# Kernel tuning notes

Hardware: AMD Instinct MI355X
Metric: run time of the kernel (lower is better)

The kernel has to match this reference:

```python
import jax, jax.numpy as jnp
import numpy as np

DIM_IN = 512
DIM_HEAD = 64
HEADS = 8
KV_HEADS = 2
CONTEXT_LEN = 4096
B, N = 4, 2048


def setup_inputs() -> dict:
    key = jax.random.key(0)
    ks = jax.random.split(key, 6)
    s = 1.0 / np.sqrt(DIM_IN)
    return {
        "x": jax.random.normal(ks[0], (B, DIM_IN, N), dtype=jnp.float32),
        "gamma": jnp.ones((DIM_IN,), jnp.float32),
        "beta": jnp.zeros((DIM_IN,), jnp.float32),
        "Wq": jax.random.normal(ks[1], (DIM_IN, DIM_HEAD * HEADS), jnp.float32) * s,
        "Wkv": jax.random.normal(ks[2], (DIM_IN, DIM_HEAD * KV_HEADS * 2), jnp.float32) * s,
        "Wout": jax.random.normal(ks[3], (DIM_HEAD * HEADS, DIM_IN), jnp.float32) * (1.0 / np.sqrt(DIM_HEAD * HEADS)),
        "bout": jnp.zeros((DIM_IN,), jnp.float32),
    }


def _rotate_half(t):
    t1, t2 = jnp.split(t, 2, axis=-1)
    return jnp.concatenate([-t2, t1], axis=-1)


def _xpos_rotary(q, k, n, dim_head, scale_base):
    # lucidrains-style xPos rotary embedding
    pos = jnp.arange(n, dtype=jnp.float32)
    inv_freq = 1.0 / (10000.0 ** (jnp.arange(0, dim_head, 2, dtype=jnp.float32) / dim_head))
    freqs = pos[:, None] * inv_freq[None, :]            # (n, dh/2)
    freqs = jnp.concatenate([freqs, freqs], axis=-1)    # (n, dh)
    base_scale = (jnp.arange(0, dim_head, 2, dtype=jnp.float32) + 0.4 * dim_head) / (1.4 * dim_head)
    power = (pos - n // 2) / scale_base                 # (n,)
    scale = base_scale[None, :] ** power[:, None]       # (n, dh/2)
    scale = jnp.concatenate([scale, scale], axis=-1)    # (n, dh)
    cos, sin = jnp.cos(freqs), jnp.sin(freqs)
    q = (q * cos + _rotate_half(q) * sin) * scale
    k = (k * cos + _rotate_half(k) * sin) / scale
    return q, k


def reference(x, gamma, beta, Wq, Wkv, Wout, bout):
    b, d, n = x.shape
    h, kvh, dh = HEADS, KV_HEADS, DIM_HEAD
    xt = jnp.swapaxes(x, 1, 2)                           # (b, n, d)
    mu = jnp.mean(xt, axis=-1, keepdims=True)
    var = jnp.mean((xt - mu) ** 2, axis=-1, keepdims=True)
    xn = (xt - mu) * jax.lax.rsqrt(var + 1e-5) * gamma + beta
    q = (xn @ Wq).reshape(b, n, h, dh).transpose(0, 2, 1, 3)      # (b, h, n, dh)
    kv = xn @ Wkv
    k, v = jnp.split(kv, 2, axis=-1)
    k = k.reshape(b, n, kvh, dh).transpose(0, 2, 1, 3)            # (b, kvh, n, dh)
    v = v.reshape(b, n, kvh, dh).transpose(0, 2, 1, 3)
    r = h // kvh
    # repeat 'b h n d -> b (r h) n d': tile whole kv-head block r times
    k = jnp.tile(k, (1, r, 1, 1))
    v = jnp.tile(v, (1, r, 1, 1))
    q, k = _xpos_rotary(q, k, n, dh, CONTEXT_LEN)
    scores = jnp.einsum("bhqd,bhkd->bhqk", q, k) * (1.0 / np.sqrt(dh))
    attn = jax.nn.softmax(scores, axis=-1)
    out = jnp.einsum("bhqk,bhkd->bhqd", attn, v)                  # (b, h, n, dh)
    out = out.transpose(0, 2, 1, 3).reshape(b, n, h * dh)
    y = xn + out @ Wout + bout                                    # residual uses normed x
    return jnp.swapaxes(y, 1, 2)                                  # (b, d, n)
```

## Files before the change

### kernel.cpp

```cpp
#include <hip/hip_runtime.h>
#include <stdint.h>

#define DIM 512
#define DH  64
#define NH  8
#define NKV 2
#define NB  4
#define NS  2048
#define TAB (NS*32)

typedef __attribute__((ext_vector_type(8))) short short8;
typedef __attribute__((ext_vector_type(4))) short s16x4;
typedef __attribute__((ext_vector_type(4))) float f32x4;
typedef __attribute__((ext_vector_type(16))) float f32x16;
typedef __attribute__((ext_vector_type(2))) unsigned uint2v;
typedef __attribute__((ext_vector_type(4))) unsigned uint4v;

__device__ __forceinline__ unsigned short f2bf(float f) {
  union { float f; unsigned u; } v; v.f = f;
  return (unsigned short)((v.u + 0x7fffu + ((v.u >> 16) & 1u)) >> 16);
}
__device__ __forceinline__ float bf2f(unsigned short b) {
  union { unsigned u; float f; } v; v.u = ((unsigned)b) << 16;
  return v.f;
}
__device__ __forceinline__ unsigned cvt_pk_bf16(float a, float b) {
  unsigned r;
  asm("v_cvt_pk_bf16_f32 %0, %1, %2" : "=v"(r) : "v"(a), "v"(b));
  return r;
}
__device__ __forceinline__ float exp2_raw(float x) {
  float r;
  asm("v_exp_f32 %0, %1" : "=v"(r) : "v"(x));
  return r;
}
__device__ __forceinline__ float rcp_raw(float x) {
  float r;
  asm("v_rcp_f32 %0, %1" : "=v"(r) : "v"(x));
  return r;
}
__device__ __forceinline__ short8 merge8(short8 a, short8 b, float rl) {
  uint4v u;
  #pragma unroll
  for (int i = 0; i < 4; ++i) {
    float x0 = (bf2f((unsigned short)a[2*i])   + bf2f((unsigned short)b[2*i]))   * rl;
    float x1 = (bf2f((unsigned short)a[2*i+1]) + bf2f((unsigned short)b[2*i+1])) * rl;
    u[i] = cvt_pk_bf16(x0, x1);
  }
  return __builtin_bit_cast(short8, u);
}

__global__ __launch_bounds__(256) void lnprep_kernel(const float* __restrict__ x,
    const float* __restrict__ gamma, const float* __restrict__ beta,
    const float* __restrict__ Wq, const float* __restrict__ Wkv, const float* __restrict__ Wout,
    unsigned short* __restrict__ xn, unsigned short* __restrict__ Wqkvt,
    unsigned short* __restrict__ Woutt, float* __restrict__ tabs) {
  __shared__ float t[64][65];
  const int gid = blockIdx.x;
  const int tid = threadIdx.x;
  if (gid < 256) {
    const int b = gid >> 6;
    const int n0 = (gid & 63) * 32;
    const int nl = tid & 31, grp = tid >> 5;
    const float* xb = x + (size_t)b * DIM * NS + (size_t)grp * 64 * NS + n0 + nl;
    float v[64];
    float s = 0.f, s2 = 0.f;
    #pragma unroll
    for (int i = 0; i < 64; ++i) {
      v[i] = xb[(size_t)i * NS];
      s += v[i]; s2 += v[i] * v[i];
    }
    float* sm = &t[0][0];
    float* sq = &t[8][0];
    float* mu_s = &t[16][0];
    float* rs_s = &t[17][0];
    sm[grp*32 + nl] = s; sq[grp*32 + nl] = s2;
    __syncthreads();
    if (tid < 32) {
      float ts = 0.f, ts2 = 0.f;
      #pragma unroll
      for (int g = 0; g < 8; ++g) { ts += sm[g*32 + tid]; ts2 += sq[g*32 + tid]; }
      float mu = ts * (1.f/512.f);
      float var = ts2 * (1.f/512.f) - mu*mu;
      mu_s[tid] = mu; rs_s[tid] = rsqrtf(var + 1e-5f);
    }
    __syncthreads();
    const float mu = mu_s[nl], rs = rs_s[nl];
    unsigned short* dst = &xn[((size_t)(b*NS + n0 + nl))*DIM + grp*64];
    #pragma unroll
    for (int c = 0; c < 8; ++c) {
      short8 o;
      #pragma unroll
      for (int j = 0; j < 8; ++j) {
        int d = grp*64 + c*8 + j;
        o[j] = (short)f2bf((v[c*8 + j] - mu) * rs * gamma[d] + beta[d]);
      }
      *(short8*)&dst[c*8] = o;
    }
    return;
  }
  const int id = gid - 256;
  if (id >= 160) {
    int base = (id - 160) * 256 + tid;
    #pragma unroll 4
    for (int ii = 0; ii < 32; ++ii) {
      int tix = base + ii * 2048;
      int pos = tix >> 5, i = tix & 31;
      float inv = exp2f(-(float)i * (13.287712379549449f / 32.f));
      float ang = (float)pos * inv;
      float sv, cv; sincosf(ang, &sv, &cv);
      float bse = ((float)(2*i) + 25.6f) / 89.6f;
      float power = ((float)pos - 1024.f) / 4096.f;
      float sc = exp2f(power * log2f(bse));
      tabs[tix]         = cv;
      tabs[TAB + tix]   = sv;
      tabs[2*TAB + tix] = sc * 0.125f * 1.4426950408889634f;
      tabs[3*TAB + tix] = 1.f / sc;
    }
    return;
  }
  const float* src; int W, k0, c0; unsigned short* dst; int drow0;
  if (id < 64)      { src = Wq;  W = 512; k0 = (id>>3)*64;        c0 = (id&7)*64;        dst = Wqkvt; drow0 = c0; }
  else if (id < 96) { int i2 = id-64; src = Wkv; W = 256; k0 = (i2>>2)*64; c0 = (i2&3)*64; dst = Wqkvt; drow0 = 512 + c0; }
  else              { int i3 = id-96; src = Wout; W = 512; k0 = (i3>>3)*64; c0 = (i3&7)*64; dst = Woutt; drow0 = c0; }
  #pragma unroll 4
  for (int it = 0; it < 16; ++it) {
    int row = it*4 + (tid>>6), col = tid & 63;
    t[row][col] = src[(size_t)(k0+row)*W + c0 + col];
  }
  __syncthreads();
  #pragma unroll 4
  for (int it = 0; it < 16; ++it) {
    int row = it*4 + (tid>>6), col = tid & 63;
    dst[(size_t)(drow0 + row)*512 + k0 + col] = f2bf(t[col][row]);
  }
}

__global__ __launch_bounds__(256, 3) void qkv_kernel(const unsigned short* __restrict__ A,
    const unsigned short* __restrict__ Bt, const float* __restrict__ tabs,
    unsigned short* __restrict__ q, unsigned short* __restrict__ k,
    unsigned short* __restrict__ v) {
  __shared__ __align__(16) short As[2][64][40];
  __shared__ __align__(16) short Bs[2][128][40];
  const int m0 = blockIdx.x * 64, ntile = blockIdx.y, n0 = ntile * 128;
  const int tid = threadIdx.x, w = tid >> 6, lane = tid & 63;
  const int wr = w >> 1, wc = w & 1;
  f32x4 acc[2][4];
  #pragma unroll
  for (int i = 0; i < 2; ++i)
    #pragma unroll
    for (int j = 0; j < 4; ++j) acc[i][j] = (f32x4){0.f,0.f,0.f,0.f};
  const int rA = tid >> 2, c8 = (tid & 3) * 8;
  const unsigned short* Ar0 = &A[(size_t)(m0 + rA)*DIM + c8];
  const unsigned short* Br0 = &Bt[(size_t)(n0 + rA)*DIM + c8];
  const unsigned short* Br1 = &Bt[(size_t)(n0 + 64 + rA)*DIM + c8];
  *(short8*)&As[0][rA][c8]      = *(const short8*)Ar0;
  *(short8*)&Bs[0][rA][c8]      = *(const short8*)Br0;
  *(short8*)&Bs[0][64 + rA][c8] = *(const short8*)Br1;
  short8 pa0 = *(const short8*)(Ar0 + 32);
  short8 pb0 = *(const short8*)(Br0 + 32);
  short8 pb1 = *(const short8*)(Br1 + 32);
  __syncthreads();
  for (int t = 0; t < 16; ++t) {
    const int cur = t & 1;
    short8 af[2], bfr[4];
    #pragma unroll
    for (int mf = 0; mf < 2; ++mf)
      af[mf] = *(const short8*)&As[cur][wr*32 + mf*16 + (lane & 15)][(lane >> 4)*8];
    #pragma unroll
    for (int nf = 0; nf < 4; ++nf)
      bfr[nf] = *(const short8*)&Bs[cur][wc*64 + nf*16 + (lane & 15)][(lane >> 4)*8];
    __builtin_amdgcn_s_setprio(1);
    #pragma unroll
    for (int mf = 0; mf < 2; ++mf)
      #pragma unroll
      for (int nf = 0; nf < 4; ++nf)
        acc[mf][nf] = __builtin_amdgcn_mfma_f32_16x16x32_bf16(af[mf], bfr[nf], acc[mf][nf], 0, 0, 0);
    __builtin_amdgcn_s_setprio(0);
    if (t < 15) {
      *(short8*)&As[cur^1][rA][c8]      = pa0;
      *(short8*)&Bs[cur^1][rA][c8]      = pb0;
      *(short8*)&Bs[cur^1][64 + rA][c8] = pb1;
      if (t < 14) {
        const int kc = (t + 2) * 32;
        pa0 = *(const short8*)(Ar0 + kc);
        pb0 = *(const short8*)(Br0 + kc);
        pb1 = *(const short8*)(Br1 + kc);
      }
      __syncthreads();
    }
  }
  const int mw = m0 + wr*32, cw = n0 + wc*64;
  if (ntile < 4) {
    #pragma unroll
    for (int nfp = 0; nfp < 2; ++nfp) {
      const int c_lo = cw + nfp*16 + (lane & 15);
      const int head = c_lo >> 6, ii = c_lo & 31;
      const float* tb = tabs + ii;
      #pragma unroll
      for (int mf = 0; mf < 2; ++mf) {
        #pragma unroll
        for (int r = 0; r < 4; ++r) {
          int mm = mw + mf*16 + (lane >> 4)*4 + r;
          int bb = mm >> 11, n = mm & (NS-1);
          float cv = tb[n*32], sv = tb[TAB + n*32], qs = tb[2*TAB + n*32];
          float lo = acc[mf][nfp][r], hi = acc[mf][nfp+2][r];
          size_t base = (((size_t)bb*NH + head)*NS + n)*DH;
          q[base + ii]      = f2bf((lo*cv - hi*sv)*qs);
          q[base + ii + 32] = f2bf((hi*cv + lo*sv)*qs);
        }
      }
    }
  } else if (ntile == 4) {
    #pragma unroll
    for (int nfp = 0; nfp < 2; ++nfp) {
      const int c_lo = cw + nfp*16 + (lane & 15);
      const int kvh = (c_lo - 512) >> 6, ii = c_lo & 31;
      const float* tb = tabs + ii;
      #pragma unroll
      for (int mf = 0; mf < 2; ++mf) {
        #pragma unroll
        for (int r = 0; r < 4; ++r) {
          int mm = mw + mf*16 + (lane >> 4)*4 + r;
          int bb = mm >> 11, n = mm & (NS-1);
          float cv = tb[n*32], sv = tb[TAB + n*32], ks = tb[3*TAB + n*32];
          float lo = acc[mf][nfp][r], hi = acc[mf][nfp+2][r];
          size_t base = (((size_t)bb*NKV + kvh)*NS + n)*DH;
          k[base + ii]      = f2bf((lo*cv - hi*sv)*ks);
          k[base + ii + 32] = f2bf((hi*cv + lo*sv)*ks);
        }
      }
    }
  } else {
    #pragma unroll
    for (int nf = 0; nf < 4; ++nf) {
      const int c = cw + nf*16 + (lane & 15);
      const int rel = c - 640;
      const int kvh = rel >> 6, dd = rel & 63;
      #pragma unroll
      for (int mf = 0; mf < 2; ++mf) {
        int mm = mw + mf*16 + (lane >> 4)*4;
        int bb = mm >> 11, n = mm & (NS-1);
        s16x4 sv4;
        #pragma unroll
        for (int r = 0; r < 4; ++r) sv4[r] = (short)f2bf(acc[mf][nf][r]);
        *(s16x4*)&v[(((size_t)bb*NKV + kvh)*DH + dd)*NS + n] = sv4;
      }
    }
  }
}

__global__ __launch_bounds__(512, 2) void attn_kernel(const unsigned short* __restrict__ q,
    const unsigned short* __restrict__ kg, const unsigned short* __restrict__ vtp,
    unsigned short* __restrict__ op0, unsigned short* __restrict__ op1,
    float* __restrict__ lp) {
  __shared__ __align__(16) short kt[2][64][72];
  __shared__ __align__(16) short vt[2][64][72];
  const int bid = blockIdx.x;
  const int dsr = (bid & 7) * 64 + (bid >> 3);
  const int qt   = dsr & 7;
  const int half = (dsr >> 3) & 1;
  const int bh   = dsr >> 4;
  const int h = bh & 7, b = bh >> 3;
  const int kvh = h & (NKV-1);
  const int q0 = qt * 256;
  const int tid = threadIdx.x, w = tid >> 6, lane = tid & 63;
  const int l31 = lane & 31, hf = lane >> 5;
  short8 q8[4];
  const unsigned short* qp = q + (((size_t)b*NH + h)*NS + q0 + w*32 + l31)*DH + hf*8;
  #pragma unroll
  for (int s = 0; s < 4; ++s) q8[s] = *(const short8*)(qp + s*16);
  const unsigned short* kb = kg + ((size_t)b*NKV + kvh)*NS*DH;
  const unsigned short* vb = vtp + ((size_t)b*NKV + kvh)*DH*NS;
  const int kbase = half * 1024;
  const int srow = tid >> 3, scol = (tid & 7) * 8;
  *(short8*)&kt[0][srow][scol] = *(const short8*)&kb[(size_t)(kbase + srow)*DH + scol];
  *(short8*)&vt[0][srow][scol] = *(const short8*)&vb[(size_t)srow*NS + kbase + scol];
  short8 kr = *(const short8*)&kb[(size_t)(kbase + 64 + srow)*DH + scol];
  short8 vr = *(const short8*)&vb[(size_t)srow*NS + kbase + 64 + scol];
  f32x16 o0 = {}, o1 = {};
  float lsum = 0.f;
  __syncthreads();
  for (int t = 0; t < 16; ++t) {
    const int cur = t & 1;
    short8 kf0[4], kf1[4];
    #pragma unroll
    for (int s = 0; s < 4; ++s) {
      kf0[s] = *(const short8*)&kt[cur][l31][s*16 + hf*8];
      kf1[s] = *(const short8*)&kt[cur][32 + l31][s*16 + hf*8];
    }
    f32x16 st0 = {}, st1 = {};
    __builtin_amdgcn_s_setprio(1);
    #pragma unroll
    for (int s = 0; s < 4; ++s) {
      st0 = __builtin_amdgcn_mfma_f32_32x32x16_bf16(kf0[s], q8[s], st0, 0, 0, 0);
      st1 = __builtin_amdgcn_mfma_f32_32x32x16_bf16(kf1[s], q8[s], st1, 0, 0, 0);
    }
    __builtin_amdgcn_s_setprio(0);
    float p0[16], p1[16];
    #pragma unroll
    for (int r = 0; r < 16; ++r) {
      p0[r] = exp2_raw(st0[r]);
      p1[r] = exp2_raw(st1[r]);
      lsum += p0[r] + p1[r];
    }
    short8 paf[4];
    #pragma unroll
    for (int t2 = 0; t2 < 2; ++t2) {
      const float* pp = t2 ? p1 : p0;
      #pragma unroll
      for (int w16 = 0; w16 < 2; ++w16) {
        const int rb = w16*8;
        unsigned x = cvt_pk_bf16(pp[rb+0], pp[rb+1]);
        unsigned z = cvt_pk_bf16(pp[rb+2], pp[rb+3]);
        unsigned y = cvt_pk_bf16(pp[rb+4], pp[rb+5]);
        unsigned u = cvt_pk_bf16(pp[rb+6], pp[rb+7]);
        uint2v r1 = __builtin_amdgcn_permlane32_swap(x, y, false, false);
        uint2v r2 = __builtin_amdgcn_permlane32_swap(z, u, false, false);
        uint4v pk4;
        pk4[0] = r1[0]; pk4[1] = r2[0]; pk4[2] = r1[1]; pk4[3] = r2[1];
        paf[t2*2 + w16] = __builtin_bit_cast(short8, pk4);
      }
    }
    __builtin_amdgcn_s_setprio(1);
    #pragma unroll
    for (int kwin = 0; kwin < 4; ++kwin) {
      short8 vf0 = *(const short8*)&vt[cur][l31][kwin*16 + hf*8];
      short8 vf1 = *(const short8*)&vt[cur][32 + l31][kwin*16 + hf*8];
      o0 = __builtin_amdgcn_mfma_f32_32x32x16_bf16(paf[kwin], vf0, o0, 0, 0, 0);
      o1 = __builtin_amdgcn_mfma_f32_32x32x16_bf16(paf[kwin], vf1, o1, 0, 0, 0);
    }
    __builtin_amdgcn_s_setprio(0);
    if (t < 15) {
      *(short8*)&kt[cur^1][srow][scol] = kr;
      *(short8*)&vt[cur^1][srow][scol] = vr;
      if (t < 14) {
        const int k2 = kbase + (t + 2) * 64;
        kr = *(const short8*)&kb[(size_t)(k2 + srow)*DH + scol];
        vr = *(const short8*)&vb[(size_t)srow*NS + k2 + scol];
      }
      __syncthreads();
    }
  }
  lsum += __shfl_xor(lsum, 32);
  if (hf == 0)
    lp[(size_t)half*NB*NH*NS + ((size_t)b*NH + h)*NS + q0 + w*32 + l31] = lsum;
  unsigned short* op = half ? op1 : op0;
  #pragma unroll
  for (int r = 0; r < 16; ++r) {
    const int ql = (r & 3) + 8*(r >> 2) + 4*hf;
    const int n = q0 + w*32 + ql;
    unsigned short* aor = &op[((size_t)b*NS + n)*DIM + h*DH + l31];
    aor[0]  = f2bf(o0[r]);
    aor[32] = f2bf(o1[r]);
  }
}

__global__ __launch_bounds__(256, 3) void out_kernel(const unsigned short* __restrict__ op0,
    const unsigned short* __restrict__ op1, const float* __restrict__ lp,
    const unsigned short* __restrict__ Bt, const unsigned short* __restrict__ xn,
    const float* __restrict__ bout, float* __restrict__ out) {
  __shared__ __align__(16) short As[2][64][40];
  __shared__ __align__(16) short Bs[2][128][40];
  const int m0 = blockIdx.x * 64, n0 = blockIdx.y * 128;
  const int tid = threadIdx.x, w = tid >> 6, lane = tid & 63;
  const int wr = w >> 1, wc = w & 1;
  f32x4 acc[2][4];
  #pragma unroll
  for (int i = 0; i < 2; ++i)
    #pragma unroll
    for (int j = 0; j < 4; ++j) acc[i][j] = (f32x4){0.f,0.f,0.f,0.f};
  const int rA = tid >> 2, c8 = (tid & 3) * 8;
  const int rowm = m0 + rA;
  const int b0 = rowm >> 11, nn0 = rowm & (NS-1);
  const float* lp0 = lp + ((size_t)b0*NH)*NS + nn0;
  const float* lp1 = lp0 + (size_t)NB*NH*NS;
  const unsigned short* A0 = &op0[(size_t)rowm*DIM + c8];
  const unsigned short* A1 = &op1[(size_t)rowm*DIM + c8];
  const unsigned short* Br0 = &Bt[(size_t)(n0 + rA)*DIM + c8];
  const unsigned short* Br1 = &Bt[(size_t)(n0 + 64 + rA)*DIM + c8];
  float rlc = rcp_raw(lp0[0] + lp1[0]);
  *(short8*)&As[0][rA][c8]      = merge8(*(const short8*)A0, *(const short8*)A1, rlc);
  *(short8*)&Bs[0][rA][c8]      = *(const short8*)Br0;
  *(short8*)&Bs[0][64 + rA][c8] = *(const short8*)Br1;
  short8 pa0 = *(const short8*)(A0 + 32);
  short8 pa1 = *(const short8*)(A1 + 32);
  float rlp = rlc;
  short8 pb0 = *(const short8*)(Br0 + 32);
  short8 pb1 = *(const short8*)(Br1 + 32);
  __syncthreads();
  for (int t = 0; t < 16; ++t) {
    const int cur = t & 1;
    short8 af[2], bfr[4];
    #pragma unroll
    for (int mf = 0; mf < 2; ++mf)
      af[mf] = *(const short8*)&As[cur][wr*32 + mf*16 + (lane & 15)][(lane >> 4)*8];
    #pragma unroll
    for (int nf = 0; nf < 4; ++nf)
      bfr[nf] = *(const short8*)&Bs[cur][wc*64 + nf*16 + (lane & 15)][(lane >> 4)*8];
    __builtin_amdgcn_s_setprio(1);
    #pragma unroll
    for (int mf = 0; mf < 2; ++mf)
      #pragma unroll
      for (int nf = 0; nf < 4; ++nf)
        acc[mf][nf] = __builtin_amdgcn_mfma_f32_16x16x32_bf16(af[mf], bfr[nf], acc[mf][nf], 0, 0, 0);
    __builtin_amdgcn_s_setprio(0);
    if (t < 15) {
      *(short8*)&As[cur^1][rA][c8]      = merge8(pa0, pa1, rlp);
      *(short8*)&Bs[cur^1][rA][c8]      = pb0;
      *(short8*)&Bs[cur^1][64 + rA][c8] = pb1;
      if (t < 14) {
        const int kc = (t + 2) * 32;
        pa0 = *(const short8*)(A0 + kc);
        pa1 = *(const short8*)(A1 + kc);
        pb0 = *(const short8*)(Br0 + kc);
        pb1 = *(const short8*)(Br1 + kc);
        const int h2 = (t + 2) >> 1;
        rlp = rcp_raw(lp0[h2*NS] + lp1[h2*NS]);
      }
      __syncthreads();
    }
  }
  const int mw = m0 + wr*32, cw = n0 + wc*64;
  #pragma unroll
  for (int nf = 0; nf < 4; ++nf) {
    const int d = cw + nf*16 + (lane & 15);
    const float bo = bout[d];
    #pragma unroll
    for (int mf = 0; mf < 2; ++mf) {
      const int mb = mw + mf*16 + (lane >> 4)*4;
      const int bb = mb >> 11, n = mb & (NS-1);
      f32x4 res;
      #pragma unroll
      for (int r = 0; r < 4; ++r)
        res[r] = acc[mf][nf][r] + bf2f(xn[(size_t)(mb + r)*DIM + d]) + bo;
      *(f32x4*)&out[((size_t)bb*DIM + d)*NS + n] = res;
    }
  }
}

extern "C" void kernel_launch(void* const* d_in, const int* in_sizes, int n_in,
                              void* d_out, int out_size, void* d_ws, size_t ws_size,
                              hipStream_t stream) {
  (void)in_sizes; (void)n_in; (void)out_size; (void)ws_size;
  const float* x     = (const float*)d_in[0];
  const float* gamma = (const float*)d_in[1];
  const float* beta  = (const float*)d_in[2];
  const float* Wq    = (const float*)d_in[3];
  const float* Wkv   = (const float*)d_in[4];
  const float* Wout  = (const float*)d_in[5];
  const float* bout  = (const float*)d_in[6];
  float* out = (float*)d_out;
  char* ws = (char*)d_ws;
  unsigned short* xn    = (unsigned short*)(ws);
  unsigned short* qb    = (unsigned short*)(ws + (size_t)(8<<20));
  unsigned short* kb    = (unsigned short*)(ws + (size_t)(16<<20));
  unsigned short* vb    = (unsigned short*)(ws + (size_t)(18<<20));
  unsigned short* op0   = (unsigned short*)(ws + (size_t)(20<<20));
  unsigned short* op1   = (unsigned short*)(ws + (size_t)(28<<20));
  unsigned short* wqkvt = (unsigned short*)(ws + (size_t)(36<<20));
  unsigned short* woutt = (unsigned short*)(ws + (size_t)(36<<20) + 786432);
  float* tabs           = (float*)(ws + (size_t)(36<<20) + 786432 + 524288);
  float* lp             = (float*)(ws + (size_t)(36<<20) + 786432 + 524288 + 1048576);

  lnprep_kernel<<<dim3(424), dim3(256), 0, stream>>>(x, gamma, beta, Wq, Wkv, Wout,
                                                     xn, wqkvt, woutt, tabs);
  qkv_kernel<<<dim3(128, 6), dim3(256), 0, stream>>>(xn, wqkvt, tabs, qb, kb, vb);
  attn_kernel<<<dim3(512), dim3(512), 0, stream>>>(qb, kb, vb, op0, op1, lp);
  out_kernel<<<dim3(128, 4), dim3(256), 0, stream>>>(op0, op1, lp, woutt, xn, bout, out);
}
```

Measured before the change: 85.34 us.

## Split attention key range into four partitions and merge four partials in output GEMM

The attention kernel now splits each query tile's keys into four 512-key quarters instead of two halves. This doubles the block count to 1024, and each block loops 8 key tiles instead of 16. The output projection kernel merges four bf16 partial outputs and four row-sum partials before normalising. This adds more parallelism and shorter per-block latency, but costs extra workspace traffic for two more 8MB partial buffers and extra loads in the out kernel. The launch bound is raised to 8 blocks per CU, which may cap registers hard enough to cause spills.

```diff
diff --git a/kernel.cpp b/kernel.cpp
--- a/kernel.cpp
+++ b/kernel.cpp
@@ -39,12 +39,14 @@
   asm("v_rcp_f32 %0, %1" : "=v"(r) : "v"(x));
   return r;
 }
-__device__ __forceinline__ short8 merge8(short8 a, short8 b, float rl) {
+__device__ __forceinline__ short8 merge8x4(short8 a, short8 b, short8 c, short8 d, float rl) {
   uint4v u;
   #pragma unroll
   for (int i = 0; i < 4; ++i) {
-    float x0 = (bf2f((unsigned short)a[2*i])   + bf2f((unsigned short)b[2*i]))   * rl;
-    float x1 = (bf2f((unsigned short)a[2*i+1]) + bf2f((unsigned short)b[2*i+1])) * rl;
+    float x0 = ((bf2f((unsigned short)a[2*i])   + bf2f((unsigned short)b[2*i]))
+              + (bf2f((unsigned short)c[2*i])   + bf2f((unsigned short)d[2*i]))) * rl;
+    float x1 = ((bf2f((unsigned short)a[2*i+1]) + bf2f((unsigned short)b[2*i+1]))
+              + (bf2f((unsigned short)c[2*i+1]) + bf2f((unsigned short)d[2*i+1]))) * rl;
     u[i] = cvt_pk_bf16(x0, x1);
   }
   return __builtin_bit_cast(short8, u);
@@ -250,17 +252,18 @@
   }
 }
 
-__global__ __launch_bounds__(512, 2) void attn_kernel(const unsigned short* __restrict__ q,
+__global__ __launch_bounds__(512, 8) void attn_kernel(const unsigned short* __restrict__ q,
     const unsigned short* __restrict__ kg, const unsigned short* __restrict__ vtp,
     unsigned short* __restrict__ op0, unsigned short* __restrict__ op1,
+    unsigned short* __restrict__ op2, unsigned short* __restrict__ op3,
     float* __restrict__ lp) {
   __shared__ __align__(16) short kt[2][64][72];
   __shared__ __align__(16) short vt[2][64][72];
   const int bid = blockIdx.x;
-  const int dsr = (bid & 7) * 64 + (bid >> 3);
-  const int qt   = dsr & 7;
-  const int half = (dsr >> 3) & 1;
-  const int bh   = dsr >> 4;
+  const int dsr = (bid & 7) * 128 + (bid >> 3);
+  const int qt      = dsr & 7;
+  const int quarter = (dsr >> 3) & 3;
+  const int bh      = dsr >> 5;
   const int h = bh & 7, b = bh >> 3;
   const int kvh = h & (NKV-1);
   const int q0 = qt * 256;
@@ -272,7 +275,7 @@
   for (int s = 0; s < 4; ++s) q8[s] = *(const short8*)(qp + s*16);
   const unsigned short* kb = kg + ((size_t)b*NKV + kvh)*NS*DH;
   const unsigned short* vb = vtp + ((size_t)b*NKV + kvh)*DH*NS;
-  const int kbase = half * 1024;
+  const int kbase = quarter * 512;
   const int srow = tid >> 3, scol = (tid & 7) * 8;
   *(short8*)&kt[0][srow][scol] = *(const short8*)&kb[(size_t)(kbase + srow)*DH + scol];
   *(short8*)&vt[0][srow][scol] = *(const short8*)&vb[(size_t)srow*NS + kbase + scol];
@@ -281,7 +284,7 @@
   f32x16 o0 = {}, o1 = {};
   float lsum = 0.f;
   __syncthreads();
-  for (int t = 0; t < 16; ++t) {
+  for (int t = 0; t < 8; ++t) {
     const int cur = t & 1;
     short8 kf0[4], kf1[4];
     #pragma unroll
@@ -331,10 +334,10 @@
       o1 = __builtin_amdgcn_mfma_f32_32x32x16_bf16(paf[kwin], vf1, o1, 0, 0, 0);
     }
     __builtin_amdgcn_s_setprio(0);
-    if (t < 15) {
+    if (t < 7) {
       *(short8*)&kt[cur^1][srow][scol] = kr;
       *(short8*)&vt[cur^1][srow][scol] = vr;
-      if (t < 14) {
+      if (t < 6) {
         const int k2 = kbase + (t + 2) * 64;
         kr = *(const short8*)&kb[(size_t)(k2 + srow)*DH + scol];
         vr = *(const short8*)&vb[(size_t)srow*NS + k2 + scol];
@@ -344,8 +347,9 @@
   }
   lsum += __shfl_xor(lsum, 32);
   if (hf == 0)
-    lp[(size_t)half*NB*NH*NS + ((size_t)b*NH + h)*NS + q0 + w*32 + l31] = lsum;
-  unsigned short* op = half ? op1 : op0;
+    lp[(size_t)quarter*NB*NH*NS + ((size_t)b*NH + h)*NS + q0 + w*32 + l31] = lsum;
+  unsigned short* op = (quarter & 2) ? ((quarter & 1) ? op3 : op2)
+                                     : ((quarter & 1) ? op1 : op0);
   #pragma unroll
   for (int r = 0; r < 16; ++r) {
     const int ql = (r & 3) + 8*(r >> 2) + 4*hf;
@@ -357,7 +361,8 @@
 }
 
 __global__ __launch_bounds__(256, 3) void out_kernel(const unsigned short* __restrict__ op0,
-    const unsigned short* __restrict__ op1, const float* __restrict__ lp,
+    const unsigned short* __restrict__ op1, const unsigned short* __restrict__ op2,
+    const unsigned short* __restrict__ op3, const float* __restrict__ lp,
     const unsigned short* __restrict__ Bt, const unsigned short* __restrict__ xn,
     const float* __restrict__ bout, float* __restrict__ out) {
   __shared__ __align__(16) short As[2][64][40];
@@ -373,18 +378,23 @@
   const int rA = tid >> 2, c8 = (tid & 3) * 8;
   const int rowm = m0 + rA;
   const int b0 = rowm >> 11, nn0 = rowm & (NS-1);
+  const size_t lstride = (size_t)NB*NH*NS;
   const float* lp0 = lp + ((size_t)b0*NH)*NS + nn0;
-  const float* lp1 = lp0 + (size_t)NB*NH*NS;
   const unsigned short* A0 = &op0[(size_t)rowm*DIM + c8];
   const unsigned short* A1 = &op1[(size_t)rowm*DIM + c8];
+  const unsigned short* A2 = &op2[(size_t)rowm*DIM + c8];
+  const unsigned short* A3 = &op3[(size_t)rowm*DIM + c8];
   const unsigned short* Br0 = &Bt[(size_t)(n0 + rA)*DIM + c8];
   const unsigned short* Br1 = &Bt[(size_t)(n0 + 64 + rA)*DIM + c8];
-  float rlc = rcp_raw(lp0[0] + lp1[0]);
-  *(short8*)&As[0][rA][c8]      = merge8(*(const short8*)A0, *(const short8*)A1, rlc);
+  float rlc = rcp_raw(((lp0[0] + lp0[lstride]) + (lp0[2*lstride] + lp0[3*lstride])));
+  *(short8*)&As[0][rA][c8] = merge8x4(*(const short8*)A0, *(const short8*)A1,
+                                      *(const short8*)A2, *(const short8*)A3, rlc);
   *(short8*)&Bs[0][rA][c8]      = *(const short8*)Br0;
   *(short8*)&Bs[0][64 + rA][c8] = *(const short8*)Br1;
   short8 pa0 = *(const short8*)(A0 + 32);
   short8 pa1 = *(const short8*)(A1 + 32);
+  short8 pa2 = *(const short8*)(A2 + 32);
+  short8 pa3 = *(const short8*)(A3 + 32);
   float rlp = rlc;
   short8 pb0 = *(const short8*)(Br0 + 32);
   short8 pb1 = *(const short8*)(Br1 + 32);
@@ -406,17 +416,20 @@
         acc[mf][nf] = __builtin_amdgcn_mfma_f32_16x16x32_bf16(af[mf], bfr[nf], acc[mf][nf], 0, 0, 0);
     __builtin_amdgcn_s_setprio(0);
     if (t < 15) {
-      *(short8*)&As[cur^1][rA][c8]      = merge8(pa0, pa1, rlp);
+      *(short8*)&As[cur^1][rA][c8]      = merge8x4(pa0, pa1, pa2, pa3, rlp);
       *(short8*)&Bs[cur^1][rA][c8]      = pb0;
       *(short8*)&Bs[cur^1][64 + rA][c8] = pb1;
       if (t < 14) {
         const int kc = (t + 2) * 32;
         pa0 = *(const short8*)(A0 + kc);
         pa1 = *(const short8*)(A1 + kc);
+        pa2 = *(const short8*)(A2 + kc);
+        pa3 = *(const short8*)(A3 + kc);
         pb0 = *(const short8*)(Br0 + kc);
         pb1 = *(const short8*)(Br1 + kc);
         const int h2 = (t + 2) >> 1;
-        rlp = rcp_raw(lp0[h2*NS] + lp1[h2*NS]);
+        rlp = rcp_raw(((lp0[h2*NS] + lp0[h2*NS + lstride])
+                     + (lp0[h2*NS + 2*lstride] + lp0[h2*NS + 3*lstride])));
       }
       __syncthreads();
     }
@@ -458,14 +471,16 @@
   unsigned short* vb    = (unsigned short*)(ws + (size_t)(18<<20));
   unsigned short* op0   = (unsigned short*)(ws + (size_t)(20<<20));
   unsigned short* op1   = (unsigned short*)(ws + (size_t)(28<<20));
-  unsigned short* wqkvt = (unsigned short*)(ws + (size_t)(36<<20));
-  unsigned short* woutt = (unsigned short*)(ws + (size_t)(36<<20) + 786432);
-  float* tabs           = (float*)(ws + (size_t)(36<<20) + 786432 + 524288);
-  float* lp             = (float*)(ws + (size_t)(36<<20) + 786432 + 524288 + 1048576);
+  unsigned short* op2   = (unsigned short*)(ws + (size_t)(36<<20));
+  unsigned short* op3   = (unsigned short*)(ws + (size_t)(44<<20));
+  unsigned short* wqkvt = (unsigned short*)(ws + (size_t)(52<<20));
+  unsigned short* woutt = (unsigned short*)(ws + (size_t)(52<<20) + 786432);
+  float* tabs           = (float*)(ws + (size_t)(52<<20) + 786432 + 524288);
+  float* lp             = (float*)(ws + (size_t)(52<<20) + 786432 + 524288 + 1048576);
 
   lnprep_kernel<<<dim3(424), dim3(256), 0, stream>>>(x, gamma, beta, Wq, Wkv, Wout,
                                                      xn, wqkvt, woutt, tabs);
   qkv_kernel<<<dim3(128, 6), dim3(256), 0, stream>>>(xn, wqkvt, tabs, qb, kb, vb);
-  attn_kernel<<<dim3(512), dim3(512), 0, stream>>>(qb, kb, vb, op0, op1, lp);
-  out_kernel<<<dim3(128, 4), dim3(256), 0, stream>>>(op0, op1, lp, woutt, xn, bout, out);
-}
+  attn_kernel<<<dim3(1024), dim3(512), 0, stream>>>(qb, kb, vb, op0, op1, op2, op3, lp);
+  out_kernel<<<dim3(128, 4), dim3(256), 0, stream>>>(op0, op1, op2, op3, lp, woutt, xn, bout, out);
+}
```

New measurement: 329.3 us. +285.9%, slower.

## Pre-swizzle K/V into MFMA fragment layout and load directly from global

Applied to the files above, without the earlier changes.

The qkv kernel now writes K and V in a layout that already matches the MFMA operand fragments, so each lane reads contiguous 16-byte chunks. The attention kernel drops its LDS double-buffering and all __syncthreads, loading K/V fragments straight from global memory (L2-cached). Blocks shrink to 256 threads and the grid doubles to 1024, and the setprio hints are removed. This removes LDS traffic and barrier stalls, but each wave now re-reads K/V from cache and global load latency is exposed without explicit prefetch.

```diff
diff --git a/kernel.cpp b/kernel.cpp
--- a/kernel.cpp
+++ b/kernel.cpp
@@ -216,6 +216,7 @@
     for (int nfp = 0; nfp < 2; ++nfp) {
       const int c_lo = cw + nfp*16 + (lane & 15);
       const int kvh = (c_lo - 512) >> 6, ii = c_lo & 31;
+      const int s_lo = ii >> 4, hfk = (ii >> 3) & 1, e = ii & 7;
       const float* tb = tabs + ii;
       #pragma unroll
       for (int mf = 0; mf < 2; ++mf) {
@@ -225,9 +226,11 @@
           int bb = mm >> 11, n = mm & (NS-1);
           float cv = tb[n*32], sv = tb[TAB + n*32], ks = tb[3*TAB + n*32];
           float lo = acc[mf][nfp][r], hi = acc[mf][nfp+2][r];
-          size_t base = (((size_t)bb*NKV + kvh)*NS + n)*DH;
-          k[base + ii]      = f2bf((lo*cv - hi*sv)*ks);
-          k[base + ii + 32] = f2bf((hi*cv + lo*sv)*ks);
+          const int hb = bb*NKV + kvh;
+          size_t cbase = (((size_t)hb*32 + (n >> 6))*2 + ((n >> 5) & 1))*4;
+          size_t lanepart = (size_t)(hfk*32 + (n & 31))*8 + e;
+          k[(cbase + s_lo)*512 + lanepart]     = f2bf((lo*cv - hi*sv)*ks);
+          k[(cbase + s_lo + 2)*512 + lanepart] = f2bf((hi*cv + lo*sv)*ks);
         }
       }
     }
@@ -237,66 +240,64 @@
       const int c = cw + nf*16 + (lane & 15);
       const int rel = c - 640;
       const int kvh = rel >> 6, dd = rel & 63;
+      const int dh2 = dd >> 5, l31v = dd & 31;
       #pragma unroll
       for (int mf = 0; mf < 2; ++mf) {
         int mm = mw + mf*16 + (lane >> 4)*4;
         int bb = mm >> 11, n = mm & (NS-1);
+        const int hb = bb*NKV + kvh;
         s16x4 sv4;
         #pragma unroll
         for (int r = 0; r < 4; ++r) sv4[r] = (short)f2bf(acc[mf][nf][r]);
-        *(s16x4*)&v[(((size_t)bb*NKV + kvh)*DH + dd)*NS + n] = sv4;
-      }
-    }
-  }
-}
-
-__global__ __launch_bounds__(512, 2) void attn_kernel(const unsigned short* __restrict__ q,
-    const unsigned short* __restrict__ kg, const unsigned short* __restrict__ vtp,
+        size_t idx = (((((size_t)hb*32 + (n >> 6))*2 + dh2)*4 + ((n >> 4) & 3))*64
+                     + ((n >> 3) & 1)*32 + l31v)*8 + (n & 7);
+        *(s16x4*)&v[idx] = sv4;
+      }
+    }
+  }
+}
+
+__global__ __launch_bounds__(256) void attn_kernel(const unsigned short* __restrict__ q,
+    const unsigned short* __restrict__ kfb, const unsigned short* __restrict__ vfb,
     unsigned short* __restrict__ op0, unsigned short* __restrict__ op1,
     float* __restrict__ lp) {
-  __shared__ __align__(16) short kt[2][64][72];
-  __shared__ __align__(16) short vt[2][64][72];
   const int bid = blockIdx.x;
-  const int dsr = (bid & 7) * 64 + (bid >> 3);
-  const int qt   = dsr & 7;
-  const int half = (dsr >> 3) & 1;
-  const int bh   = dsr >> 4;
+  const int dsr = (bid & 7) * 128 + (bid >> 3);
+  const int qtile = dsr & 15;
+  const int half  = (dsr >> 4) & 1;
+  const int bh    = dsr >> 5;
   const int h = bh & 7, b = bh >> 3;
   const int kvh = h & (NKV-1);
-  const int q0 = qt * 256;
+  const int hb = b*NKV + kvh;
   const int tid = threadIdx.x, w = tid >> 6, lane = tid & 63;
   const int l31 = lane & 31, hf = lane >> 5;
+  const int q0 = qtile*128 + w*32;
   short8 q8[4];
-  const unsigned short* qp = q + (((size_t)b*NH + h)*NS + q0 + w*32 + l31)*DH + hf*8;
+  const unsigned short* qp = q + (((size_t)b*NH + h)*NS + q0 + l31)*DH + hf*8;
   #pragma unroll
   for (int s = 0; s < 4; ++s) q8[s] = *(const short8*)(qp + s*16);
-  const unsigned short* kb = kg + ((size_t)b*NKV + kvh)*NS*DH;
-  const unsigned short* vb = vtp + ((size_t)b*NKV + kvh)*DH*NS;
-  const int kbase = half * 1024;
-  const int srow = tid >> 3, scol = (tid & 7) * 8;
-  *(short8*)&kt[0][srow][scol] = *(const short8*)&kb[(size_t)(kbase + srow)*DH + scol];
-  *(short8*)&vt[0][srow][scol] = *(const short8*)&vb[(size_t)srow*NS + kbase + scol];
-  short8 kr = *(const short8*)&kb[(size_t)(kbase + 64 + srow)*DH + scol];
-  short8 vr = *(const short8*)&vb[(size_t)srow*NS + kbase + 64 + scol];
+  const unsigned short* kf_base = kfb + ((size_t)hb*32 + half*16)*4096 + lane*8;
+  const unsigned short* vf_base = vfb + ((size_t)hb*32 + half*16)*4096 + lane*8;
   f32x16 o0 = {}, o1 = {};
   float lsum = 0.f;
-  __syncthreads();
   for (int t = 0; t < 16; ++t) {
-    const int cur = t & 1;
+    const unsigned short* kc = kf_base + (size_t)t*4096;
+    const unsigned short* vc = vf_base + (size_t)t*4096;
     short8 kf0[4], kf1[4];
     #pragma unroll
     for (int s = 0; s < 4; ++s) {
-      kf0[s] = *(const short8*)&kt[cur][l31][s*16 + hf*8];
-      kf1[s] = *(const short8*)&kt[cur][32 + l31][s*16 + hf*8];
+      kf0[s] = *(const short8*)(kc + s*512);
+      kf1[s] = *(const short8*)(kc + (4 + s)*512);
     }
     f32x16 st0 = {}, st1 = {};
-    __builtin_amdgcn_s_setprio(1);
     #pragma unroll
     for (int s = 0; s < 4; ++s) {
       st0 = __builtin_amdgcn_mfma_f32_32x32x16_bf16(kf0[s], q8[s], st0, 0, 0, 0);
       st1 = __builtin_amdgcn_mfma_f32_32x32x16_bf16(kf1[s], q8[s], st1, 0, 0, 0);
     }
-    __builtin_amdgcn_s_setprio(0);
+    short8 vf0[4];
+    #pragma unroll
+    for (int kw = 0; kw < 4; ++kw) vf0[kw] = *(const short8*)(vc + kw*512);
     float p0[16], p1[16];
     #pragma unroll
     for (int r = 0; r < 16; ++r) {
@@ -322,34 +323,24 @@
         paf[t2*2 + w16] = __builtin_bit_cast(short8, pk4);
       }
     }
-    __builtin_amdgcn_s_setprio(1);
-    #pragma unroll
-    for (int kwin = 0; kwin < 4; ++kwin) {
-      short8 vf0 = *(const short8*)&vt[cur][l31][kwin*16 + hf*8];
-      short8 vf1 = *(const short8*)&vt[cur][32 + l31][kwin*16 + hf*8];
-      o0 = __builtin_amdgcn_mfma_f32_32x32x16_bf16(paf[kwin], vf0, o0, 0, 0, 0);
-      o1 = __builtin_amdgcn_mfma_f32_32x32x16_bf16(paf[kwin], vf1, o1, 0, 0, 0);
-    }
-    __builtin_amdgcn_s_setprio(0);
-    if (t < 15) {
-      *(short8*)&kt[cur^1][srow][scol] = kr;
-      *(short8*)&vt[cur^1][srow][scol] = vr;
-      if (t < 14) {
-        const int k2 = kbase + (t + 2) * 64;
-        kr = *(const short8*)&kb[(size_t)(k2 + srow)*DH + scol];
-        vr = *(const short8*)&vb[(size_t)srow*NS + k2 + scol];
-      }
-      __syncthreads();
-    }
+    short8 vf1[4];
+    #pragma unroll
+    for (int kw = 0; kw < 4; ++kw) vf1[kw] = *(const short8*)(vc + (4 + kw)*512);
+    #pragma unroll
+    for (int kw = 0; kw < 4; ++kw)
+      o0 = __builtin_amdgcn_mfma_f32_32x32x16_bf16(paf[kw], vf0[kw], o0, 0, 0, 0);
+    #pragma unroll
+    for (int kw = 0; kw < 4; ++kw)
+      o1 = __builtin_amdgcn_mfma_f32_32x32x16_bf16(paf[kw], vf1[kw], o1, 0, 0, 0);
   }
   lsum += __shfl_xor(lsum, 32);
   if (hf == 0)
-    lp[(size_t)half*NB*NH*NS + ((size_t)b*NH + h)*NS + q0 + w*32 + l31] = lsum;
+    lp[(size_t)half*NB*NH*NS + ((size_t)b*NH + h)*NS + q0 + l31] = lsum;
   unsigned short* op = half ? op1 : op0;
   #pragma unroll
   for (int r = 0; r < 16; ++r) {
     const int ql = (r & 3) + 8*(r >> 2) + 4*hf;
-    const int n = q0 + w*32 + ql;
+    const int n = q0 + ql;
     unsigned short* aor = &op[((size_t)b*NS + n)*DIM + h*DH + l31];
     aor[0]  = f2bf(o0[r]);
     aor[32] = f2bf(o1[r]);
@@ -454,8 +445,8 @@
   char* ws = (char*)d_ws;
   unsigned short* xn    = (unsigned short*)(ws);
   unsigned short* qb    = (unsigned short*)(ws + (size_t)(8<<20));
-  unsigned short* kb    = (unsigned short*)(ws + (size_t)(16<<20));
-  unsigned short* vb    = (unsigned short*)(ws + (size_t)(18<<20));
+  unsigned short* kfb   = (unsigned short*)(ws + (size_t)(16<<20));
+  unsigned short* vfb   = (unsigned short*)(ws + (size_t)(18<<20));
   unsigned short* op0   = (unsigned short*)(ws + (size_t)(20<<20));
   unsigned short* op1   = (unsigned short*)(ws + (size_t)(28<<20));
   unsigned short* wqkvt = (unsigned short*)(ws + (size_t)(36<<20));
@@ -465,7 +456,7 @@
 
   lnprep_kernel<<<dim3(424), dim3(256), 0, stream>>>(x, gamma, beta, Wq, Wkv, Wout,
                                                      xn, wqkvt, woutt, tabs);
-  qkv_kernel<<<dim3(128, 6), dim3(256), 0, stream>>>(xn, wqkvt, tabs, qb, kb, vb);
-  attn_kernel<<<dim3(512), dim3(512), 0, stream>>>(qb, kb, vb, op0, op1, lp);
+  qkv_kernel<<<dim3(128, 6), dim3(256), 0, stream>>>(xn, wqkvt, tabs, qb, kfb, vfb);
+  attn_kernel<<<dim3(1024), dim3(256), 0, stream>>>(qb, kfb, vfb, op0, op1, lp);
   out_kernel<<<dim3(128, 4), dim3(256), 0, stream>>>(op0, op1, lp, woutt, xn, bout, out);
 }
```

New measurement: 92.92 us. 8.9% more time.

## Load GEMM tiles directly into LDS with global_load_lds and XOR swizzle

Applied to the files above, without the earlier changes.

Replaces the register-staged global-to-LDS copies in the QKV and output projection GEMMs with direct global_load_lds transfers. It drops the padded LDS rows in favour of an XOR swizzle on the 16-byte column chunk to avoid bank conflicts. This removes the register round-trip and VGPR pressure of the software prefetch, at the cost of a shallower one-stage prefetch, since the next tile is issued at the start of each iteration rather than two ahead. Correctness depends on global_load_lds placing each lane's 16 bytes contiguously per wave.

```diff
diff --git a/kernel.cpp b/kernel.cpp
--- a/kernel.cpp
+++ b/kernel.cpp
@@ -16,6 +16,8 @@
 typedef __attribute__((ext_vector_type(2))) unsigned uint2v;
 typedef __attribute__((ext_vector_type(4))) unsigned uint4v;
 
+#define SWZ(r, j) ((j) ^ (((r) >> 1) & 3))
+
 __device__ __forceinline__ unsigned short f2bf(float f) {
   union { float f; unsigned u; } v; v.f = f;
   return (unsigned short)((v.u + 0x7fffu + ((v.u >> 16) & 1u)) >> 16);
@@ -38,6 +40,11 @@
   float r;
   asm("v_rcp_f32 %0, %1" : "=v"(r) : "v"(x));
   return r;
+}
+__device__ __forceinline__ void gload16(const unsigned short* g, short* l) {
+  __builtin_amdgcn_global_load_lds(
+      (const __attribute__((address_space(1))) unsigned int*)g,
+      (__attribute__((address_space(3))) unsigned int*)l, 16, 0, 0);
 }
 __device__ __forceinline__ short8 merge8(short8 a, short8 b, float rl) {
   uint4v u;
@@ -140,8 +147,8 @@
     const unsigned short* __restrict__ Bt, const float* __restrict__ tabs,
     unsigned short* __restrict__ q, unsigned short* __restrict__ k,
     unsigned short* __restrict__ v) {
-  __shared__ __align__(16) short As[2][64][40];
-  __shared__ __align__(16) short Bs[2][128][40];
+  __shared__ __align__(16) short As[2][64][32];
+  __shared__ __align__(16) short Bs[2][128][32];
   const int m0 = blockIdx.x * 64, ntile = blockIdx.y, n0 = ntile * 128;
   const int tid = threadIdx.x, w = tid >> 6, lane = tid & 63;
   const int wr = w >> 1, wc = w & 1;
@@ -150,26 +157,37 @@
   for (int i = 0; i < 2; ++i)
     #pragma unroll
     for (int j = 0; j < 4; ++j) acc[i][j] = (f32x4){0.f,0.f,0.f,0.f};
-  const int rA = tid >> 2, c8 = (tid & 3) * 8;
-  const unsigned short* Ar0 = &A[(size_t)(m0 + rA)*DIM + c8];
-  const unsigned short* Br0 = &Bt[(size_t)(n0 + rA)*DIM + c8];
-  const unsigned short* Br1 = &Bt[(size_t)(n0 + 64 + rA)*DIM + c8];
-  *(short8*)&As[0][rA][c8]      = *(const short8*)Ar0;
-  *(short8*)&Bs[0][rA][c8]      = *(const short8*)Br0;
-  *(short8*)&Bs[0][64 + rA][c8] = *(const short8*)Br1;
-  short8 pa0 = *(const short8*)(Ar0 + 32);
-  short8 pb0 = *(const short8*)(Br0 + 32);
-  short8 pb1 = *(const short8*)(Br1 + 32);
+  const int rA = tid >> 2;
+  const int cSw = SWZ(rA, (tid & 3)) * 8;
+  const unsigned short* Ag  = &A [(size_t)(m0 + rA)*DIM + cSw];
+  const unsigned short* Bg0 = &Bt[(size_t)(n0 + rA)*DIM + cSw];
+  const unsigned short* Bg1 = &Bt[(size_t)(n0 + 64 + rA)*DIM + cSw];
+  short* ldsA[2]  = { &As[0][w*16][0], &As[1][w*16][0] };
+  short* ldsBa[2] = { &Bs[0][w*16][0], &Bs[1][w*16][0] };
+  short* ldsBb[2] = { &Bs[0][64 + w*16][0], &Bs[1][64 + w*16][0] };
+  gload16(Ag,  ldsA[0]);
+  gload16(Bg0, ldsBa[0]);
+  gload16(Bg1, ldsBb[0]);
   __syncthreads();
   for (int t = 0; t < 16; ++t) {
     const int cur = t & 1;
+    if (t < 15) {
+      const int kc = (t + 1) * 32;
+      gload16(Ag + kc,  ldsA[cur ^ 1]);
+      gload16(Bg0 + kc, ldsBa[cur ^ 1]);
+      gload16(Bg1 + kc, ldsBb[cur ^ 1]);
+    }
     short8 af[2], bfr[4];
     #pragma unroll
-    for (int mf = 0; mf < 2; ++mf)
-      af[mf] = *(const short8*)&As[cur][wr*32 + mf*16 + (lane & 15)][(lane >> 4)*8];
-    #pragma unroll
-    for (int nf = 0; nf < 4; ++nf)
-      bfr[nf] = *(const short8*)&Bs[cur][wc*64 + nf*16 + (lane & 15)][(lane >> 4)*8];
+    for (int mf = 0; mf < 2; ++mf) {
+      const int ra = wr*32 + mf*16 + (lane & 15);
+      af[mf] = *(const short8*)&As[cur][ra][SWZ(ra, lane >> 4) * 8];
+    }
+    #pragma unroll
+    for (int nf = 0; nf < 4; ++nf) {
+      const int rb = wc*64 + nf*16 + (lane & 15);
+      bfr[nf] = *(const short8*)&Bs[cur][rb][SWZ(rb, lane >> 4) * 8];
+    }
     __builtin_amdgcn_s_setprio(1);
     #pragma unroll
     for (int mf = 0; mf < 2; ++mf)
@@ -177,18 +195,7 @@
       for (int nf = 0; nf < 4; ++nf)
         acc[mf][nf] = __builtin_amdgcn_mfma_f32_16x16x32_bf16(af[mf], bfr[nf], acc[mf][nf], 0, 0, 0);
     __builtin_amdgcn_s_setprio(0);
-    if (t < 15) {
-      *(short8*)&As[cur^1][rA][c8]      = pa0;
-      *(short8*)&Bs[cur^1][rA][c8]      = pb0;
-      *(short8*)&Bs[cur^1][64 + rA][c8] = pb1;
-      if (t < 14) {
-        const int kc = (t + 2) * 32;
-        pa0 = *(const short8*)(Ar0 + kc);
-        pb0 = *(const short8*)(Br0 + kc);
-        pb1 = *(const short8*)(Br1 + kc);
-      }
-      __syncthreads();
-    }
+    __syncthreads();
   }
   const int mw = m0 + wr*32, cw = n0 + wc*64;
   if (ntile < 4) {
@@ -361,7 +368,7 @@
     const unsigned short* __restrict__ Bt, const unsigned short* __restrict__ xn,
     const float* __restrict__ bout, float* __restrict__ out) {
   __shared__ __align__(16) short As[2][64][40];
-  __shared__ __align__(16) short Bs[2][128][40];
+  __shared__ __align__(16) short Bs[2][128][32];
   const int m0 = blockIdx.x * 64, n0 = blockIdx.y * 128;
   const int tid = threadIdx.x, w = tid >> 6, lane = tid & 63;
   const int wr = w >> 1, wc = w & 1;
@@ -371,33 +378,41 @@
     #pragma unroll
     for (int j = 0; j < 4; ++j) acc[i][j] = (f32x4){0.f,0.f,0.f,0.f};
   const int rA = tid >> 2, c8 = (tid & 3) * 8;
+  const int cSw = SWZ(rA, (tid & 3)) * 8;
   const int rowm = m0 + rA;
   const int b0 = rowm >> 11, nn0 = rowm & (NS-1);
   const float* lp0 = lp + ((size_t)b0*NH)*NS + nn0;
   const float* lp1 = lp0 + (size_t)NB*NH*NS;
   const unsigned short* A0 = &op0[(size_t)rowm*DIM + c8];
   const unsigned short* A1 = &op1[(size_t)rowm*DIM + c8];
-  const unsigned short* Br0 = &Bt[(size_t)(n0 + rA)*DIM + c8];
-  const unsigned short* Br1 = &Bt[(size_t)(n0 + 64 + rA)*DIM + c8];
+  const unsigned short* Bg0 = &Bt[(size_t)(n0 + rA)*DIM + cSw];
+  const unsigned short* Bg1 = &Bt[(size_t)(n0 + 64 + rA)*DIM + cSw];
+  short* ldsBa[2] = { &Bs[0][w*16][0], &Bs[1][w*16][0] };
+  short* ldsBb[2] = { &Bs[0][64 + w*16][0], &Bs[1][64 + w*16][0] };
   float rlc = rcp_raw(lp0[0] + lp1[0]);
-  *(short8*)&As[0][rA][c8]      = merge8(*(const short8*)A0, *(const short8*)A1, rlc);
-  *(short8*)&Bs[0][rA][c8]      = *(const short8*)Br0;
-  *(short8*)&Bs[0][64 + rA][c8] = *(const short8*)Br1;
+  *(short8*)&As[0][rA][c8] = merge8(*(const short8*)A0, *(const short8*)A1, rlc);
+  gload16(Bg0, ldsBa[0]);
+  gload16(Bg1, ldsBb[0]);
   short8 pa0 = *(const short8*)(A0 + 32);
   short8 pa1 = *(const short8*)(A1 + 32);
   float rlp = rlc;
-  short8 pb0 = *(const short8*)(Br0 + 32);
-  short8 pb1 = *(const short8*)(Br1 + 32);
   __syncthreads();
   for (int t = 0; t < 16; ++t) {
     const int cur = t & 1;
+    if (t < 15) {
+      const int kc = (t + 1) * 32;
+      gload16(Bg0 + kc, ldsBa[cur ^ 1]);
+      gload16(Bg1 + kc, ldsBb[cur ^ 1]);
+    }
     short8 af[2], bfr[4];
     #pragma unroll
     for (int mf = 0; mf < 2; ++mf)
       af[mf] = *(const short8*)&As[cur][wr*32 + mf*16 + (lane & 15)][(lane >> 4)*8];
     #pragma unroll
-    for (int nf = 0; nf < 4; ++nf)
-      bfr[nf] = *(const short8*)&Bs[cur][wc*64 + nf*16 + (lane & 15)][(lane >> 4)*8];
+    for (int nf = 0; nf < 4; ++nf) {
+      const int rb = wc*64 + nf*16 + (lane & 15);
+      bfr[nf] = *(const short8*)&Bs[cur][rb][SWZ(rb, lane >> 4) * 8];
+    }
     __builtin_amdgcn_s_setprio(1);
     #pragma unroll
     for (int mf = 0; mf < 2; ++mf)
@@ -406,15 +421,11 @@
         acc[mf][nf] = __builtin_amdgcn_mfma_f32_16x16x32_bf16(af[mf], bfr[nf], acc[mf][nf], 0, 0, 0);
     __builtin_amdgcn_s_setprio(0);
     if (t < 15) {
-      *(short8*)&As[cur^1][rA][c8]      = merge8(pa0, pa1, rlp);
-      *(short8*)&Bs[cur^1][rA][c8]      = pb0;
-      *(short8*)&Bs[cur^1][64 + rA][c8] = pb1;
+      *(short8*)&As[cur^1][rA][c8] = merge8(pa0, pa1, rlp);
       if (t < 14) {
-        const int kc = (t + 2) * 32;
-        pa0 = *(const short8*)(A0 + kc);
-        pa1 = *(const short8*)(A1 + kc);
-        pb0 = *(const short8*)(Br0 + kc);
-        pb1 = *(const short8*)(Br1 + kc);
+        const int kc2 = (t + 2) * 32;
+        pa0 = *(const short8*)(A0 + kc2);
+        pa1 = *(const short8*)(A1 + kc2);
         const int h2 = (t + 2) >> 1;
         rlp = rcp_raw(lp0[h2*NS] + lp1[h2*NS]);
       }
```

Result: slower. 87.66 us (+2.7%).
